# Performance work log

Measured on AMD Instinct MI355X. Metric: run time of the kernel, lower is better.

Reference implementation:

```python
import jax, jax.numpy as jnp
import numpy as np

N_NODES = 100000
N_EDGES = 3200000
D_IN, D_HID, D_OUT = 128, 128, 128


def setup_inputs() -> dict:
    key = jax.random.key(0)
    ks = jax.random.split(key, 8)
    x = jax.random.normal(ks[0], (N_NODES, D_IN), dtype=jnp.float32)
    edge_index = jax.random.randint(ks[1], (2, N_EDGES), 0, N_NODES, dtype=jnp.int64)
    def lin(k, din, dout):
        # glorot-ish init for GCNConv weight
        s = 1.0 / np.sqrt(din)
        return jax.random.uniform(k, (din, dout), jnp.float32, -s, s)
    W0 = lin(ks[2], D_IN, D_HID)
    b0 = jnp.zeros((D_HID,), jnp.float32)
    W1 = lin(ks[3], D_HID, D_HID)
    b1 = jnp.zeros((D_HID,), jnp.float32)
    W2 = lin(ks[4], D_HID, D_OUT)
    b2 = jnp.zeros((D_OUT,), jnp.float32)
    return {"x": x, "edge_index": edge_index, "W0": W0, "b0": b0,
            "W1": W1, "b1": b1, "W2": W2, "b2": b2}


def _gcn_norm(edge_index, n_nodes):
    # PyG gcn_norm with self-loops: deg over target index, sym normalization
    loop = jnp.arange(n_nodes, dtype=edge_index.dtype)
    src = jnp.concatenate([edge_index[0], loop])
    dst = jnp.concatenate([edge_index[1], loop])
    deg = jax.ops.segment_sum(jnp.ones_like(dst, dtype=jnp.float32), dst,
                              num_segments=n_nodes)
    dinv = jnp.where(deg > 0, jax.lax.rsqrt(deg), 0.0)
    norm = dinv[src] * dinv[dst]  # [E + N]
    return src, dst, norm


def _gcn_conv(h, src, dst, norm, W, b, n_nodes):
    h = h @ W                                   # [N, dout] transform first
    msg = h[src] * norm[:, None]                # gather + scale
    out = jax.ops.segment_sum(msg, dst, num_segments=n_nodes)  # scatter-add
    return out + b


def reference(x, edge_index, W0, b0, W1, b1, W2, b2):
    n = x.shape[0]
    src, dst, norm = _gcn_norm(edge_index, n)
    # layer 0
    h = jax.nn.relu(_gcn_conv(x, src, dst, norm, W0, b0, n))
    # residual middle layer (dropout is identity in eval mode)
    h = jax.nn.relu(_gcn_conv(h, src, dst, norm, W1, b1, n) + h)
    # output layer
    return _gcn_conv(h, src, dst, norm, W2, b2, n)
```

## Files before the change

kernel.cpp:

```cpp
#include <hip/hip_runtime.h>
#include <hip/hip_fp16.h>

#define D 128
#define TILE 16384
typedef unsigned long long ull;
typedef _Float16 half8 __attribute__((ext_vector_type(8)));
typedef _Float16 half4v __attribute__((ext_vector_type(4)));
typedef float f32x4 __attribute__((ext_vector_type(4)));

#define KPOS(k4) (((k4) & ~31) + ((((k4) & 15) >> 2) << 3) + ((((k4) >> 4) & 1) << 2))

__global__ void k_cnt_tiles(const int* __restrict__ ei_dst, int* __restrict__ cnt,
                            int E, int ntiles, int nb) {
  __shared__ int h[256];
  for (int i = threadIdx.x; i < nb; i += 256) h[i] = 0;
  __syncthreads();
  const int t = blockIdx.x;
  const int start = t * TILE;
  int end = start + TILE;
  if (end > E) end = E;
  for (int i = start + threadIdx.x; i < end; i += 256)
    atomicAdd(&h[__builtin_nontemporal_load(&ei_dst[i]) >> 9], 1);
  __syncthreads();
  for (int b = threadIdx.x; b < nb; b += 256)
    cnt[(size_t)b * ntiles + t] = h[b];
}

__global__ void k_tile_scan(const int* __restrict__ cnt, int* __restrict__ off,
                            int nb, int ntiles) {
  __shared__ int sd[256];
  int total = 0;
  if (threadIdx.x < nb) {
    const int* row = cnt + (size_t)threadIdx.x * ntiles;
    for (int t = 0; t < ntiles; t++) total += row[t];
  }
  sd[threadIdx.x] = total;
  __syncthreads();
  for (int o = 1; o < 256; o <<= 1) {
    int v = (threadIdx.x >= o) ? sd[threadIdx.x - o] : 0;
    __syncthreads();
    sd[threadIdx.x] += v;
    __syncthreads();
  }
  int base = sd[threadIdx.x] - total;
  if (threadIdx.x < nb) {
    const int* row = cnt + (size_t)threadIdx.x * ntiles;
    int* orow = off + (size_t)threadIdx.x * ntiles;
    int run = base;
    for (int t = 0; t < ntiles; t++) { orow[t] = run; run += row[t]; }
  }
}

__global__ void k_scatter_bucket(const int* __restrict__ ei, const int* __restrict__ off,
                                 ull* __restrict__ ebb, int E, int ntiles, int nb) {
  __shared__ int h[256];
  __shared__ int base[256];
  const int t = blockIdx.x;
  for (int i = threadIdx.x; i < nb; i += 256) {
    h[i] = 0;
    base[i] = off[(size_t)i * ntiles + t];
  }
  __syncthreads();
  const int start = t * TILE;
  int end = start + TILE;
  if (end > E) end = E;
  for (int i = start + threadIdx.x; i < end; i += 256) {
    int d = __builtin_nontemporal_load(&ei[E + i]);
    int s = __builtin_nontemporal_load(&ei[i]);
    int b = d >> 9;
    int r = atomicAdd(&h[b], 1);
    ebb[(size_t)base[b] + r] = (ull)(unsigned)s | ((ull)(unsigned)d << 32);
  }
}

__global__ void k_fill_bucket2(const ull* __restrict__ ebb, const int* __restrict__ off,
                               int* __restrict__ rowptr, float* __restrict__ dinv,
                               int* __restrict__ csr, int E, int ntiles, int nb, int N) {
  __shared__ int cnt[512];
  __shared__ int ps[256];
  const int b = blockIdx.x;
  const int tid = threadIdx.x;
  const int lo = off[(size_t)b * ntiles];
  const int hi = (b + 1 < nb) ? off[(size_t)(b + 1) * ntiles] : E;
  for (int i = tid; i < 512; i += 256) cnt[i] = 0;
  __syncthreads();
  for (int i = lo + tid; i < hi; i += 256) {
    ull q = __builtin_nontemporal_load(&ebb[i]);
    atomicAdd(&cnt[(int)(q >> 32) - (b << 9)], 1);
  }
  __syncthreads();
  int c0 = cnt[2 * tid];
  int c1 = cnt[2 * tid + 1];
  int pair = c0 + c1;
  ps[tid] = pair;
  __syncthreads();
  for (int o = 1; o < 256; o <<= 1) {
    int v = (tid >= o) ? ps[tid - o] : 0;
    __syncthreads();
    ps[tid] += v;
    __syncthreads();
  }
  int base0 = lo + ps[tid] - pair;
  int v0 = (b << 9) + 2 * tid;
  int v1 = v0 + 1;
  if (v0 < N) {
    rowptr[v0] = base0;
    dinv[v0] = rsqrtf((float)c0 + 1.0f);
  }
  if (v1 < N) {
    rowptr[v1] = base0 + c0;
    dinv[v1] = rsqrtf((float)c1 + 1.0f);
  }
  if (b == 0 && tid == 0) rowptr[N] = E;
  cnt[2 * tid] = base0;
  cnt[2 * tid + 1] = base0 + c0;
  __syncthreads();
  for (int i = lo + tid; i < hi; i += 256) {
    ull q = __builtin_nontemporal_load(&ebb[i]);
    int s = (int)(unsigned)q;
    int dl = (int)(q >> 32) - (b << 9);
    int pos = atomicAdd(&cnt[dl], 1);
    csr[pos] = s;
  }
}

template <int HALF_IN>
__launch_bounds__(256, 2)
__global__ void k_gemm_mfma(const void* __restrict__ Av, const float* __restrict__ W,
                            const float* __restrict__ dinv, __half* __restrict__ Th, int n) {
  __shared__ _Float16 Al[128 * 136];
  __shared__ _Float16 Bl[128 * 136];
  const int tid = threadIdx.x;
  const int row0 = blockIdx.x * 128;

  if (HALF_IN) {
    const _Float16* A = (const _Float16*)Av;
    for (int i = tid; i < 2048; i += 256) {
      int r = i >> 4;
      int k8 = (i & 15) << 3;
      half8 v = {0, 0, 0, 0, 0, 0, 0, 0};
      if (row0 + r < n) v = *(const half8*)&A[(size_t)(row0 + r) * D + k8];
      *(half4v*)&Al[r * 136 + KPOS(k8)]     = (half4v){v[0], v[1], v[2], v[3]};
      *(half4v*)&Al[r * 136 + KPOS(k8 + 4)] = (half4v){v[4], v[5], v[6], v[7]};
    }
  } else {
    const float* A = (const float*)Av;
    for (int i = tid; i < 4096; i += 256) {
      int r = i >> 5;
      int k4 = (i & 31) << 2;
      float4 v = make_float4(0.f, 0.f, 0.f, 0.f);
      if (row0 + r < n) v = ((const float4*)A)[(size_t)(row0 + r) * 32 + (i & 31)];
      *(half4v*)&Al[r * 136 + KPOS(k4)] =
          (half4v){(_Float16)v.x, (_Float16)v.y, (_Float16)v.z, (_Float16)v.w};
    }
  }
  for (int i = tid; i < 4096; i += 256) {
    int c = i & 127;
    int k4 = (i >> 7) << 2;
    float w0 = W[(k4 + 0) * D + c];
    float w1 = W[(k4 + 1) * D + c];
    float w2 = W[(k4 + 2) * D + c];
    float w3 = W[(k4 + 3) * D + c];
    *(half4v*)&Bl[c * 136 + KPOS(k4)] =
        (half4v){(_Float16)w0, (_Float16)w1, (_Float16)w2, (_Float16)w3};
  }
  __syncthreads();

  const int w = tid >> 6;
  const int lane = tid & 63;
  const int g = lane >> 4;
  const int q = lane & 15;

  f32x4 acc[2][8];
#pragma unroll
  for (int mt = 0; mt < 2; mt++)
#pragma unroll
    for (int nt = 0; nt < 8; nt++) acc[mt][nt] = (f32x4){0.f, 0.f, 0.f, 0.f};

#pragma unroll
  for (int kt = 0; kt < 4; kt++) {
    half8 a[2], bb[8];
#pragma unroll
    for (int mt = 0; mt < 2; mt++)
      a[mt] = *(const half8*)&Al[(w * 32 + mt * 16 + q) * 136 + kt * 32 + g * 8];
#pragma unroll
    for (int nt = 0; nt < 8; nt++)
      bb[nt] = *(const half8*)&Bl[(nt * 16 + q) * 136 + kt * 32 + g * 8];
#pragma unroll
    for (int mt = 0; mt < 2; mt++)
#pragma unroll
      for (int nt = 0; nt < 8; nt++)
        acc[mt][nt] = __builtin_amdgcn_mfma_f32_16x16x32_f16(a[mt], bb[nt], acc[mt][nt], 0, 0, 0);
  }

#pragma unroll
  for (int mt = 0; mt < 2; mt++) {
    int baseRow = row0 + w * 32 + mt * 16 + g * 4;
    float dv[4];
#pragma unroll
    for (int r = 0; r < 4; r++) dv[r] = (baseRow + r < n) ? dinv[baseRow + r] : 0.f;
#pragma unroll
    for (int nt = 0; nt < 8; nt++) {
      int col = nt * 16 + q;
#pragma unroll
      for (int r = 0; r < 4; r++) {
        int gr = baseRow + r;
        if (gr < n) Th[(size_t)gr * D + col] = (__half)(acc[mt][nt][r] * dv[r]);
      }
    }
  }
}

template <int MODE>
__launch_bounds__(256)
__global__ void k_aggregate(const int* __restrict__ rowptr, const int* __restrict__ csr,
                            const float* __restrict__ dinv, const __half* __restrict__ th,
                            const float* __restrict__ b, const __half* __restrict__ resh,
                            __half* __restrict__ outh, float* __restrict__ outf, int n) {
  const int g = threadIdx.x >> 4;
  const int l16 = threadIdx.x & 15;
  const float4* t4 = (const float4*)th;
  const float4* b4 = (const float4*)b;
  float4 bb0 = b4[l16 * 2];
  float4 bb1 = b4[l16 * 2 + 1];

  for (int node = blockIdx.x * 16 + g; node < n; node += gridDim.x * 16) {
    int beg = rowptr[node];
    int end = rowptr[node + 1];
    float dd = dinv[node];

    float a0, a1, a2, a3, a4, a5, a6, a7;
    {
      float4 raw = t4[(size_t)node * 16 + l16];
      const __half2* hp = (const __half2*)&raw;
      float2 f0 = __half22float2(hp[0]);
      float2 f1 = __half22float2(hp[1]);
      float2 f2 = __half22float2(hp[2]);
      float2 f3 = __half22float2(hp[3]);
      a0 = f0.x; a1 = f0.y; a2 = f1.x; a3 = f1.y;
      a4 = f2.x; a5 = f2.y; a6 = f3.x; a7 = f3.y;
    }

#define ACC_ROW(raw)                                  \
  {                                                   \
    const __half2* hp = (const __half2*)&(raw);       \
    float2 f0 = __half22float2(hp[0]);                \
    float2 f1 = __half22float2(hp[1]);                \
    float2 f2 = __half22float2(hp[2]);                \
    float2 f3 = __half22float2(hp[3]);                \
    a0 += f0.x; a1 += f0.y; a2 += f1.x; a3 += f1.y;   \
    a4 += f2.x; a5 += f2.y; a6 += f3.x; a7 += f3.y;   \
  }

    int j = beg;
    for (; j + 8 <= end; j += 8) {
      float4 r0, r1, r2, r3, r4, r5, r6, r7;
      {
        int s0 = __builtin_nontemporal_load(&csr[j + 0]);
        int s1 = __builtin_nontemporal_load(&csr[j + 1]);
        int s2 = __builtin_nontemporal_load(&csr[j + 2]);
        int s3 = __builtin_nontemporal_load(&csr[j + 3]);
        int s4 = __builtin_nontemporal_load(&csr[j + 4]);
        int s5 = __builtin_nontemporal_load(&csr[j + 5]);
        int s6 = __builtin_nontemporal_load(&csr[j + 6]);
        int s7 = __builtin_nontemporal_load(&csr[j + 7]);
        r0 = t4[(size_t)(unsigned)s0 * 16 + l16];
        r1 = t4[(size_t)(unsigned)s1 * 16 + l16];
        r2 = t4[(size_t)(unsigned)s2 * 16 + l16];
        r3 = t4[(size_t)(unsigned)s3 * 16 + l16];
        r4 = t4[(size_t)(unsigned)s4 * 16 + l16];
        r5 = t4[(size_t)(unsigned)s5 * 16 + l16];
        r6 = t4[(size_t)(unsigned)s6 * 16 + l16];
        r7 = t4[(size_t)(unsigned)s7 * 16 + l16];
      }
      ACC_ROW(r0) ACC_ROW(r1) ACC_ROW(r2) ACC_ROW(r3)
      ACC_ROW(r4) ACC_ROW(r5) ACC_ROW(r6) ACC_ROW(r7)
    }
    for (; j + 4 <= end; j += 4) {
      int s0 = __builtin_nontemporal_load(&csr[j + 0]);
      int s1 = __builtin_nontemporal_load(&csr[j + 1]);
      int s2 = __builtin_nontemporal_load(&csr[j + 2]);
      int s3 = __builtin_nontemporal_load(&csr[j + 3]);
      float4 r0 = t4[(size_t)(unsigned)s0 * 16 + l16];
      float4 r1 = t4[(size_t)(unsigned)s1 * 16 + l16];
      float4 r2 = t4[(size_t)(unsigned)s2 * 16 + l16];
      float4 r3 = t4[(size_t)(unsigned)s3 * 16 + l16];
      ACC_ROW(r0) ACC_ROW(r1) ACC_ROW(r2) ACC_ROW(r3)
    }
    for (; j < end; ++j) {
      int s = __builtin_nontemporal_load(&csr[j]);
      float4 r = t4[(size_t)(unsigned)s * 16 + l16];
      ACC_ROW(r)
    }
#undef ACC_ROW

    float o0 = fmaf(a0, dd, bb0.x), o1 = fmaf(a1, dd, bb0.y);
    float o2 = fmaf(a2, dd, bb0.z), o3 = fmaf(a3, dd, bb0.w);
    float o4 = fmaf(a4, dd, bb1.x), o5 = fmaf(a5, dd, bb1.y);
    float o6 = fmaf(a6, dd, bb1.z), o7 = fmaf(a7, dd, bb1.w);

    if (MODE == 1) {
      float4 raw = ((const float4*)resh)[(size_t)node * 16 + l16];
      const __half2* hp = (const __half2*)&raw;
      float2 f0 = __half22float2(hp[0]);
      float2 f1 = __half22float2(hp[1]);
      float2 f2 = __half22float2(hp[2]);
      float2 f3 = __half22float2(hp[3]);
      o0 += f0.x; o1 += f0.y; o2 += f1.x; o3 += f1.y;
      o4 += f2.x; o5 += f2.y; o6 += f3.x; o7 += f3.y;
    }
    if (MODE == 0 || MODE == 1) {
      o0 = fmaxf(o0, 0.f); o1 = fmaxf(o1, 0.f); o2 = fmaxf(o2, 0.f); o3 = fmaxf(o3, 0.f);
      o4 = fmaxf(o4, 0.f); o5 = fmaxf(o5, 0.f); o6 = fmaxf(o6, 0.f); o7 = fmaxf(o7, 0.f);
      union { __half2 h[4]; float4 f; } pk;
      pk.h[0] = __floats2half2_rn(o0, o1);
      pk.h[1] = __floats2half2_rn(o2, o3);
      pk.h[2] = __floats2half2_rn(o4, o5);
      pk.h[3] = __floats2half2_rn(o6, o7);
      ((float4*)outh)[(size_t)node * 16 + l16] = pk.f;
    } else {
      ((float4*)outf)[(size_t)node * 32 + l16 * 2] = make_float4(o0, o1, o2, o3);
      ((float4*)outf)[(size_t)node * 32 + l16 * 2 + 1] = make_float4(o4, o5, o6, o7);
    }
  }
}

extern "C" void kernel_launch(void* const* d_in, const int* in_sizes, int n_in,
                              void* d_out, int out_size, void* d_ws, size_t ws_size,
                              hipStream_t stream) {
  const float* x  = (const float*)d_in[0];
  const int*   ei = (const int*)d_in[1];
  const float* W0 = (const float*)d_in[2];
  const float* b0 = (const float*)d_in[3];
  const float* W1 = (const float*)d_in[4];
  const float* b1 = (const float*)d_in[5];
  const float* W2 = (const float*)d_in[6];
  const float* b2 = (const float*)d_in[7];
  float* out = (float*)d_out;

  const int N = in_sizes[0] / D;
  const int E = in_sizes[1] / 2;

  const int ntiles = (E + TILE - 1) / TILE;
  const int nb = (N + 511) >> 9;

  char* wsb = (char*)d_ws;
  auto alloc = [&](size_t bytes) {
    char* p = wsb;
    wsb += ((bytes + 255) & ~(size_t)255);
    return p;
  };
  int*    rowptr = (int*)alloc((N + 1) * 4);
  float*  dinv   = (float*)alloc(N * 4);
  int*    cnt    = (int*)alloc((size_t)nb * ntiles * 4);
  int*    off    = (int*)alloc((size_t)nb * ntiles * 4);
  ull*    ebb    = (ull*)alloc((size_t)E * 8);
  int*    csr    = (int*)alloc((size_t)E * 4);
  __half* th     = (__half*)alloc((size_t)N * D * 2);
  __half* g1h    = (__half*)alloc((size_t)N * D * 2);
  __half* g2h    = (__half*)alloc((size_t)N * D * 2);

  dim3 b256(256);
  int gGem = (N + 127) / 128;
  int gAgg = 2048;

  k_cnt_tiles<<<ntiles, b256, 0, stream>>>(ei + E, cnt, E, ntiles, nb);
  k_tile_scan<<<1, b256, 0, stream>>>(cnt, off, nb, ntiles);
  k_scatter_bucket<<<ntiles, b256, 0, stream>>>(ei, off, ebb, E, ntiles, nb);
  k_fill_bucket2<<<nb, b256, 0, stream>>>(ebb, off, rowptr, dinv, csr, E, ntiles, nb, N);

  k_gemm_mfma<0><<<gGem, b256, 0, stream>>>(x, W0, dinv, th, N);
  k_aggregate<0><<<gAgg, b256, 0, stream>>>(rowptr, csr, dinv, th, b0, nullptr, g1h, nullptr, N);

  k_gemm_mfma<1><<<gGem, b256, 0, stream>>>(g1h, W1, dinv, th, N);
  k_aggregate<1><<<gAgg, b256, 0, stream>>>(rowptr, csr, dinv, th, b1, g1h, g2h, nullptr, N);

  k_gemm_mfma<1><<<gGem, b256, 0, stream>>>(g2h, W2, dinv, th, N);
  k_aggregate<2><<<gAgg, b256, 0, stream>>>(rowptr, csr, dinv, th, b2, nullptr, nullptr, out, N);
}
```

Before: 665.4 us.

## Pack bucket edges to 32 bits, pre-pack weights, one-node-per-group aggregation

Edge bucket entries shrink from 64-bit pairs to 32-bit words, with the source in the low 23 bits and the destination's local offset in the high 9 bits. This halves scatter and fill traffic but assumes node ids fit in 23 bits. Weights are converted once to fp16 in the MFMA-friendly layout by a small prep kernel, and the GEMM reads B fragments directly from global memory, which drops the B shared-memory tile and raises the occupancy hint. The aggregation kernel becomes non-persistent, launching one 16-lane group per node across a full grid instead of a grid-stride loop.

```diff
diff --git a/kernel.cpp b/kernel.cpp
--- a/kernel.cpp
+++ b/kernel.cpp
@@ -52,7 +52,7 @@
 }
 
 __global__ void k_scatter_bucket(const int* __restrict__ ei, const int* __restrict__ off,
-                                 ull* __restrict__ ebb, int E, int ntiles, int nb) {
+                                 unsigned* __restrict__ ebb, int E, int ntiles, int nb) {
   __shared__ int h[256];
   __shared__ int base[256];
   const int t = blockIdx.x;
@@ -69,11 +69,11 @@
     int s = __builtin_nontemporal_load(&ei[i]);
     int b = d >> 9;
     int r = atomicAdd(&h[b], 1);
-    ebb[(size_t)base[b] + r] = (ull)(unsigned)s | ((ull)(unsigned)d << 32);
-  }
-}
-
-__global__ void k_fill_bucket2(const ull* __restrict__ ebb, const int* __restrict__ off,
+    ebb[(size_t)base[b] + r] = (unsigned)s | ((unsigned)(d & 511) << 23);
+  }
+}
+
+__global__ void k_fill_bucket2(const unsigned* __restrict__ ebb, const int* __restrict__ off,
                                int* __restrict__ rowptr, float* __restrict__ dinv,
                                int* __restrict__ csr, int E, int ntiles, int nb, int N) {
   __shared__ int cnt[512];
@@ -85,8 +85,8 @@
   for (int i = tid; i < 512; i += 256) cnt[i] = 0;
   __syncthreads();
   for (int i = lo + tid; i < hi; i += 256) {
-    ull q = __builtin_nontemporal_load(&ebb[i]);
-    atomicAdd(&cnt[(int)(q >> 32) - (b << 9)], 1);
+    unsigned q = __builtin_nontemporal_load(&ebb[i]);
+    atomicAdd(&cnt[q >> 23], 1);
   }
   __syncthreads();
   int c0 = cnt[2 * tid];
@@ -116,20 +116,29 @@
   cnt[2 * tid + 1] = base0 + c0;
   __syncthreads();
   for (int i = lo + tid; i < hi; i += 256) {
-    ull q = __builtin_nontemporal_load(&ebb[i]);
-    int s = (int)(unsigned)q;
-    int dl = (int)(q >> 32) - (b << 9);
-    int pos = atomicAdd(&cnt[dl], 1);
-    csr[pos] = s;
+    unsigned q = __builtin_nontemporal_load(&ebb[i]);
+    int pos = atomicAdd(&cnt[q >> 23], 1);
+    csr[pos] = (int)(q & 0x7FFFFFu);
+  }
+}
+
+__global__ void k_prep_w(const float* __restrict__ W, _Float16* __restrict__ Wp) {
+  for (int idx = blockIdx.x * 1024 + threadIdx.x; idx < 16384; idx += 16 * 1024) {
+  }
+  int t = blockIdx.x * 256 + threadIdx.x;
+  for (int e = 0; e < 4; e++) {
+    int idx = t + e * 4096;
+    int c = idx & 127;
+    int k = idx >> 7;
+    Wp[c * 128 + KPOS(k & ~3) + (k & 3)] = (_Float16)W[k * D + c];
   }
 }
 
 template <int HALF_IN>
-__launch_bounds__(256, 2)
-__global__ void k_gemm_mfma(const void* __restrict__ Av, const float* __restrict__ W,
+__launch_bounds__(256, 3)
+__global__ void k_gemm_mfma(const void* __restrict__ Av, const _Float16* __restrict__ Wp,
                             const float* __restrict__ dinv, __half* __restrict__ Th, int n) {
   __shared__ _Float16 Al[128 * 136];
-  __shared__ _Float16 Bl[128 * 136];
   const int tid = threadIdx.x;
   const int row0 = blockIdx.x * 128;
 
@@ -154,16 +163,6 @@
           (half4v){(_Float16)v.x, (_Float16)v.y, (_Float16)v.z, (_Float16)v.w};
     }
   }
-  for (int i = tid; i < 4096; i += 256) {
-    int c = i & 127;
-    int k4 = (i >> 7) << 2;
-    float w0 = W[(k4 + 0) * D + c];
-    float w1 = W[(k4 + 1) * D + c];
-    float w2 = W[(k4 + 2) * D + c];
-    float w3 = W[(k4 + 3) * D + c];
-    *(half4v*)&Bl[c * 136 + KPOS(k4)] =
-        (half4v){(_Float16)w0, (_Float16)w1, (_Float16)w2, (_Float16)w3};
-  }
   __syncthreads();
 
   const int w = tid >> 6;
@@ -185,7 +184,7 @@
       a[mt] = *(const half8*)&Al[(w * 32 + mt * 16 + q) * 136 + kt * 32 + g * 8];
 #pragma unroll
     for (int nt = 0; nt < 8; nt++)
-      bb[nt] = *(const half8*)&Bl[(nt * 16 + q) * 136 + kt * 32 + g * 8];
+      bb[nt] = *(const half8*)&Wp[(nt * 16 + q) * 128 + kt * 32 + g * 8];
 #pragma unroll
     for (int mt = 0; mt < 2; mt++)
 #pragma unroll
@@ -217,29 +216,27 @@
                             const float* __restrict__ dinv, const __half* __restrict__ th,
                             const float* __restrict__ b, const __half* __restrict__ resh,
                             __half* __restrict__ outh, float* __restrict__ outf, int n) {
-  const int g = threadIdx.x >> 4;
+  int node = blockIdx.x * 16 + (threadIdx.x >> 4);
+  if (node >= n) return;
   const int l16 = threadIdx.x & 15;
+
+  int beg = rowptr[node];
+  int end = rowptr[node + 1];
+  float dd = dinv[node];
+
   const float4* t4 = (const float4*)th;
-  const float4* b4 = (const float4*)b;
-  float4 bb0 = b4[l16 * 2];
-  float4 bb1 = b4[l16 * 2 + 1];
-
-  for (int node = blockIdx.x * 16 + g; node < n; node += gridDim.x * 16) {
-    int beg = rowptr[node];
-    int end = rowptr[node + 1];
-    float dd = dinv[node];
-
-    float a0, a1, a2, a3, a4, a5, a6, a7;
-    {
-      float4 raw = t4[(size_t)node * 16 + l16];
-      const __half2* hp = (const __half2*)&raw;
-      float2 f0 = __half22float2(hp[0]);
-      float2 f1 = __half22float2(hp[1]);
-      float2 f2 = __half22float2(hp[2]);
-      float2 f3 = __half22float2(hp[3]);
-      a0 = f0.x; a1 = f0.y; a2 = f1.x; a3 = f1.y;
-      a4 = f2.x; a5 = f2.y; a6 = f3.x; a7 = f3.y;
-    }
+
+  float a0, a1, a2, a3, a4, a5, a6, a7;
+  {
+    float4 raw = t4[(size_t)node * 16 + l16];
+    const __half2* hp = (const __half2*)&raw;
+    float2 f0 = __half22float2(hp[0]);
+    float2 f1 = __half22float2(hp[1]);
+    float2 f2 = __half22float2(hp[2]);
+    float2 f3 = __half22float2(hp[3]);
+    a0 = f0.x; a1 = f0.y; a2 = f1.x; a3 = f1.y;
+    a4 = f2.x; a5 = f2.y; a6 = f3.x; a7 = f3.y;
+  }
 
 #define ACC_ROW(raw)                                  \
   {                                                   \
@@ -252,76 +249,78 @@
     a4 += f2.x; a5 += f2.y; a6 += f3.x; a7 += f3.y;   \
   }
 
-    int j = beg;
-    for (; j + 8 <= end; j += 8) {
-      float4 r0, r1, r2, r3, r4, r5, r6, r7;
-      {
-        int s0 = __builtin_nontemporal_load(&csr[j + 0]);
-        int s1 = __builtin_nontemporal_load(&csr[j + 1]);
-        int s2 = __builtin_nontemporal_load(&csr[j + 2]);
-        int s3 = __builtin_nontemporal_load(&csr[j + 3]);
-        int s4 = __builtin_nontemporal_load(&csr[j + 4]);
-        int s5 = __builtin_nontemporal_load(&csr[j + 5]);
-        int s6 = __builtin_nontemporal_load(&csr[j + 6]);
-        int s7 = __builtin_nontemporal_load(&csr[j + 7]);
-        r0 = t4[(size_t)(unsigned)s0 * 16 + l16];
-        r1 = t4[(size_t)(unsigned)s1 * 16 + l16];
-        r2 = t4[(size_t)(unsigned)s2 * 16 + l16];
-        r3 = t4[(size_t)(unsigned)s3 * 16 + l16];
-        r4 = t4[(size_t)(unsigned)s4 * 16 + l16];
-        r5 = t4[(size_t)(unsigned)s5 * 16 + l16];
-        r6 = t4[(size_t)(unsigned)s6 * 16 + l16];
-        r7 = t4[(size_t)(unsigned)s7 * 16 + l16];
-      }
-      ACC_ROW(r0) ACC_ROW(r1) ACC_ROW(r2) ACC_ROW(r3)
-      ACC_ROW(r4) ACC_ROW(r5) ACC_ROW(r6) ACC_ROW(r7)
-    }
-    for (; j + 4 <= end; j += 4) {
+  int j = beg;
+  for (; j + 8 <= end; j += 8) {
+    float4 r0, r1, r2, r3, r4, r5, r6, r7;
+    {
       int s0 = __builtin_nontemporal_load(&csr[j + 0]);
       int s1 = __builtin_nontemporal_load(&csr[j + 1]);
       int s2 = __builtin_nontemporal_load(&csr[j + 2]);
       int s3 = __builtin_nontemporal_load(&csr[j + 3]);
-      float4 r0 = t4[(size_t)(unsigned)s0 * 16 + l16];
-      float4 r1 = t4[(size_t)(unsigned)s1 * 16 + l16];
-      float4 r2 = t4[(size_t)(unsigned)s2 * 16 + l16];
-      float4 r3 = t4[(size_t)(unsigned)s3 * 16 + l16];
-      ACC_ROW(r0) ACC_ROW(r1) ACC_ROW(r2) ACC_ROW(r3)
+      int s4 = __builtin_nontemporal_load(&csr[j + 4]);
+      int s5 = __builtin_nontemporal_load(&csr[j + 5]);
+      int s6 = __builtin_nontemporal_load(&csr[j + 6]);
+      int s7 = __builtin_nontemporal_load(&csr[j + 7]);
+      r0 = t4[(size_t)(unsigned)s0 * 16 + l16];
+      r1 = t4[(size_t)(unsigned)s1 * 16 + l16];
+      r2 = t4[(size_t)(unsigned)s2 * 16 + l16];
+      r3 = t4[(size_t)(unsigned)s3 * 16 + l16];
+      r4 = t4[(size_t)(unsigned)s4 * 16 + l16];
+      r5 = t4[(size_t)(unsigned)s5 * 16 + l16];
+      r6 = t4[(size_t)(unsigned)s6 * 16 + l16];
+      r7 = t4[(size_t)(unsigned)s7 * 16 + l16];
     }
-    for (; j < end; ++j) {
-      int s = __builtin_nontemporal_load(&csr[j]);
-      float4 r = t4[(size_t)(unsigned)s * 16 + l16];
-      ACC_ROW(r)
-    }
+    ACC_ROW(r0) ACC_ROW(r1) ACC_ROW(r2) ACC_ROW(r3)
+    ACC_ROW(r4) ACC_ROW(r5) ACC_ROW(r6) ACC_ROW(r7)
+  }
+  for (; j + 4 <= end; j += 4) {
+    int s0 = __builtin_nontemporal_load(&csr[j + 0]);
+    int s1 = __builtin_nontemporal_load(&csr[j + 1]);
+    int s2 = __builtin_nontemporal_load(&csr[j + 2]);
+    int s3 = __builtin_nontemporal_load(&csr[j + 3]);
+    float4 r0 = t4[(size_t)(unsigned)s0 * 16 + l16];
+    float4 r1 = t4[(size_t)(unsigned)s1 * 16 + l16];
+    float4 r2 = t4[(size_t)(unsigned)s2 * 16 + l16];
+    float4 r3 = t4[(size_t)(unsigned)s3 * 16 + l16];
+    ACC_ROW(r0) ACC_ROW(r1) ACC_ROW(r2) ACC_ROW(r3)
+  }
+  for (; j < end; ++j) {
+    int s = __builtin_nontemporal_load(&csr[j]);
+    float4 r = t4[(size_t)(unsigned)s * 16 + l16];
+    ACC_ROW(r)
+  }
 #undef ACC_ROW
 
-    float o0 = fmaf(a0, dd, bb0.x), o1 = fmaf(a1, dd, bb0.y);
-    float o2 = fmaf(a2, dd, bb0.z), o3 = fmaf(a3, dd, bb0.w);
-    float o4 = fmaf(a4, dd, bb1.x), o5 = fmaf(a5, dd, bb1.y);
-    float o6 = fmaf(a6, dd, bb1.z), o7 = fmaf(a7, dd, bb1.w);
-
-    if (MODE == 1) {
-      float4 raw = ((const float4*)resh)[(size_t)node * 16 + l16];
-      const __half2* hp = (const __half2*)&raw;
-      float2 f0 = __half22float2(hp[0]);
-      float2 f1 = __half22float2(hp[1]);
-      float2 f2 = __half22float2(hp[2]);
-      float2 f3 = __half22float2(hp[3]);
-      o0 += f0.x; o1 += f0.y; o2 += f1.x; o3 += f1.y;
-      o4 += f2.x; o5 += f2.y; o6 += f3.x; o7 += f3.y;
-    }
-    if (MODE == 0 || MODE == 1) {
-      o0 = fmaxf(o0, 0.f); o1 = fmaxf(o1, 0.f); o2 = fmaxf(o2, 0.f); o3 = fmaxf(o3, 0.f);
-      o4 = fmaxf(o4, 0.f); o5 = fmaxf(o5, 0.f); o6 = fmaxf(o6, 0.f); o7 = fmaxf(o7, 0.f);
-      union { __half2 h[4]; float4 f; } pk;
-      pk.h[0] = __floats2half2_rn(o0, o1);
-      pk.h[1] = __floats2half2_rn(o2, o3);
-      pk.h[2] = __floats2half2_rn(o4, o5);
-      pk.h[3] = __floats2half2_rn(o6, o7);
-      ((float4*)outh)[(size_t)node * 16 + l16] = pk.f;
-    } else {
-      ((float4*)outf)[(size_t)node * 32 + l16 * 2] = make_float4(o0, o1, o2, o3);
-      ((float4*)outf)[(size_t)node * 32 + l16 * 2 + 1] = make_float4(o4, o5, o6, o7);
-    }
+  const float4* b4 = (const float4*)b;
+  float4 bb0 = b4[l16 * 2];
+  float4 bb1 = b4[l16 * 2 + 1];
+  float o0 = fmaf(a0, dd, bb0.x), o1 = fmaf(a1, dd, bb0.y);
+  float o2 = fmaf(a2, dd, bb0.z), o3 = fmaf(a3, dd, bb0.w);
+  float o4 = fmaf(a4, dd, bb1.x), o5 = fmaf(a5, dd, bb1.y);
+  float o6 = fmaf(a6, dd, bb1.z), o7 = fmaf(a7, dd, bb1.w);
+
+  if (MODE == 1) {
+    float4 raw = ((const float4*)resh)[(size_t)node * 16 + l16];
+    const __half2* hp = (const __half2*)&raw;
+    float2 f0 = __half22float2(hp[0]);
+    float2 f1 = __half22float2(hp[1]);
+    float2 f2 = __half22float2(hp[2]);
+    float2 f3 = __half22float2(hp[3]);
+    o0 += f0.x; o1 += f0.y; o2 += f1.x; o3 += f1.y;
+    o4 += f2.x; o5 += f2.y; o6 += f3.x; o7 += f3.y;
+  }
+  if (MODE == 0 || MODE == 1) {
+    o0 = fmaxf(o0, 0.f); o1 = fmaxf(o1, 0.f); o2 = fmaxf(o2, 0.f); o3 = fmaxf(o3, 0.f);
+    o4 = fmaxf(o4, 0.f); o5 = fmaxf(o5, 0.f); o6 = fmaxf(o6, 0.f); o7 = fmaxf(o7, 0.f);
+    union { __half2 h[4]; float4 f; } pk;
+    pk.h[0] = __floats2half2_rn(o0, o1);
+    pk.h[1] = __floats2half2_rn(o2, o3);
+    pk.h[2] = __floats2half2_rn(o4, o5);
+    pk.h[3] = __floats2half2_rn(o6, o7);
+    ((float4*)outh)[(size_t)node * 16 + l16] = pk.f;
+  } else {
+    ((float4*)outf)[(size_t)node * 32 + l16 * 2] = make_float4(o0, o1, o2, o3);
+    ((float4*)outf)[(size_t)node * 32 + l16 * 2 + 1] = make_float4(o4, o5, o6, o7);
   }
 }
 
@@ -350,31 +349,38 @@
     wsb += ((bytes + 255) & ~(size_t)255);
     return p;
   };
-  int*    rowptr = (int*)alloc((N + 1) * 4);
-  float*  dinv   = (float*)alloc(N * 4);
-  int*    cnt    = (int*)alloc((size_t)nb * ntiles * 4);
-  int*    off    = (int*)alloc((size_t)nb * ntiles * 4);
-  ull*    ebb    = (ull*)alloc((size_t)E * 8);
-  int*    csr    = (int*)alloc((size_t)E * 4);
-  __half* th     = (__half*)alloc((size_t)N * D * 2);
-  __half* g1h    = (__half*)alloc((size_t)N * D * 2);
-  __half* g2h    = (__half*)alloc((size_t)N * D * 2);
+  int*      rowptr = (int*)alloc((N + 1) * 4);
+  float*    dinv   = (float*)alloc(N * 4);
+  int*      cnt    = (int*)alloc((size_t)nb * ntiles * 4);
+  int*      off    = (int*)alloc((size_t)nb * ntiles * 4);
+  unsigned* ebb    = (unsigned*)alloc((size_t)E * 4);
+  int*      csr    = (int*)alloc((size_t)E * 4);
+  _Float16* Wp0    = (_Float16*)alloc(16384 * 2);
+  _Float16* Wp1    = (_Float16*)alloc(16384 * 2);
+  _Float16* Wp2    = (_Float16*)alloc(16384 * 2);
+  __half*   th     = (__half*)alloc((size_t)N * D * 2);
+  __half*   g1h    = (__half*)alloc((size_t)N * D * 2);
+  __half*   g2h    = (__half*)alloc((size_t)N * D * 2);
 
   dim3 b256(256);
   int gGem = (N + 127) / 128;
-  int gAgg = 2048;
+  int gAgg = (N + 15) / 16;
+
+  k_prep_w<<<16, b256, 0, stream>>>(W0, Wp0);
+  k_prep_w<<<16, b256, 0, stream>>>(W1, Wp1);
+  k_prep_w<<<16, b256, 0, stream>>>(W2, Wp2);
 
   k_cnt_tiles<<<ntiles, b256, 0, stream>>>(ei + E, cnt, E, ntiles, nb);
   k_tile_scan<<<1, b256, 0, stream>>>(cnt, off, nb, ntiles);
   k_scatter_bucket<<<ntiles, b256, 0, stream>>>(ei, off, ebb, E, ntiles, nb);
   k_fill_bucket2<<<nb, b256, 0, stream>>>(ebb, off, rowptr, dinv, csr, E, ntiles, nb, N);
 
-  k_gemm_mfma<0><<<gGem, b256, 0, stream>>>(x, W0, dinv, th, N);
+  k_gemm_mfma<0><<<gGem, b256, 0, stream>>>(x, Wp0, dinv, th, N);
   k_aggregate<0><<<gAgg, b256, 0, stream>>>(rowptr, csr, dinv, th, b0, nullptr, g1h, nullptr, N);
 
-  k_gemm_mfma<1><<<gGem, b256, 0, stream>>>(g1h, W1, dinv, th, N);
+  k_gemm_mfma<1><<<gGem, b256, 0, stream>>>(g1h, Wp1, dinv, th, N);
   k_aggregate<1><<<gAgg, b256, 0, stream>>>(rowptr, csr, dinv, th, b1, g1h, g2h, nullptr, N);
 
-  k_gemm_mfma<1><<<gGem, b256, 0, stream>>>(g2h, W2, dinv, th, N);
+  k_gemm_mfma<1><<<gGem, b256, 0, stream>>>(g2h, Wp2, dinv, th, N);
   k_aggregate<2><<<gAgg, b256, 0, stream>>>(rowptr, csr, dinv, th, b2, nullptr, nullptr, out, N);
 }
```

Measured after the change: 676.0 us. Within noise of the previous version (+1.6%).
